# Optimization experiments

Measured on AMD Instinct MI355X. Metric: run time of the kernel, lower is better.

The kernel has to match this reference:

```python
import jax, jax.numpy as jnp
import numpy as np

DIM = 64  # matches init kwarg `dim`; temperature = sqrt(DIM)


def setup_inputs() -> dict:
    key = jax.random.key(0)
    kq, kk, kv = jax.random.split(key, 3)
    B, Lq, Lk, d = 16, 4096, 4096, DIM
    q = jax.random.normal(kq, (B, Lq, d), dtype=jnp.float32)
    k = jax.random.normal(kk, (B, Lk, d), dtype=jnp.float32)
    v = jax.random.normal(kv, (B, Lk, d), dtype=jnp.float32)
    return {"q": q, "k": k, "v": v}


def reference(q, k, v):
    # attn = softmax(q @ k^T / sqrt(dim)); dropout is identity in eval mode.
    temperature = jnp.asarray(np.sqrt(DIM), dtype=q.dtype)
    scores = jnp.einsum('bqd,bkd->bqk', q, k) / temperature  # [B, Lq, Lk]
    attn = jax.nn.softmax(scores, axis=-1)
    out = jnp.einsum('bqk,bkd->bqd', attn, v)  # [B, Lq, d]
    return out
```

## Files before the change

### kernel.cpp

```cpp
#include <hip/hip_runtime.h>
#include <stdint.h>
#include <math.h>

typedef __attribute__((ext_vector_type(2)))  float f2;
typedef __attribute__((ext_vector_type(4)))  float f4;
typedef __attribute__((ext_vector_type(16))) float f32x16;
typedef __attribute__((ext_vector_type(8)))  short bf16x8;

#define NB   16
#define LSEQ 4096
#define DH   64
#define QB   128
#define KVB  64
#define NT   (LSEQ / KVB)

__device__ __forceinline__ short f2bf(float f) {
    union { float f; uint32_t u; } v; v.f = f;
    return (short)((v.u + 0x7FFFu + ((v.u >> 16) & 1u)) >> 16);
}

__device__ __forceinline__ uint32_t cvtpk(float lo, float hi) {
    uint32_t r;
    asm("v_cvt_pk_bf16_f32 %0, %1, %2" : "=v"(r) : "v"(lo), "v"(hi));
    return r;
}

__global__ __launch_bounds__(256, 2) void fa_fwd(
    const float* __restrict__ Q, const float* __restrict__ K,
    const float* __restrict__ V, float* __restrict__ O)
{
    __shared__ __align__(16) short k_lds[2][KVB * DH];
    __shared__ __align__(16) short v_lds[2][DH * KVB];

    const int tid  = threadIdx.x;
    const int lane = tid & 63;
    const int w    = tid >> 6;
    const int l31  = lane & 31;
    const int H    = lane >> 5;

    const int b  = blockIdx.x >> 5;
    const int qt = blockIdx.x & 31;
    const int q0 = qt * QB + w * 32;

    const float* Qb = Q + (size_t)b * LSEQ * DH;
    const float* Kb = K + (size_t)b * LSEQ * DH;
    const float* Vb = V + (size_t)b * LSEQ * DH;
    float*       Ob = O + (size_t)b * LSEQ * DH;

    const float QS = 0.125f * 1.44269504088896340736f;

    bf16x8 qf[4];
#pragma unroll
    for (int kb = 0; kb < 4; ++kb) {
        const float* src = Qb + (size_t)(q0 + l31) * DH + 16 * kb + 8 * H;
        f4 a = *(const f4*)src;
        f4 c = *(const f4*)(src + 4);
        bf16x8 f;
        f[0] = f2bf(a[0] * QS); f[1] = f2bf(a[1] * QS);
        f[2] = f2bf(a[2] * QS); f[3] = f2bf(a[3] * QS);
        f[4] = f2bf(c[0] * QS); f[5] = f2bf(c[1] * QS);
        f[6] = f2bf(c[2] * QS); f[7] = f2bf(c[3] * QS);
        qf[kb] = f;
    }

    f4 kreg[4];
    f2 vreg[8];

    const int k_kv0 = (tid >> 3);
    const int k_d0  = (tid & 7) * 8;
    const int v_d0  = (tid & 31) * 2;
    const int v_g   = tid >> 5;

#define LOADK(KV0)                                                              \
    {                                                                           \
        _Pragma("unroll")                                                       \
        for (int p = 0; p < 2; ++p) {                                           \
            const float* src = Kb + (size_t)((KV0) + k_kv0 + 32 * p) * DH + k_d0; \
            kreg[2 * p]     = *(const f4*)src;                                  \
            kreg[2 * p + 1] = *(const f4*)(src + 4);                            \
        }                                                                       \
        _Pragma("unroll")                                                       \
        for (int j = 0; j < 8; ++j)                                             \
            vreg[j] = *(const f2*)&Vb[(size_t)((KV0) + 8 * v_g + j) * DH + v_d0]; \
    }

#define WRITEK(BUF)                                                             \
    {                                                                           \
        _Pragma("unroll")                                                       \
        for (int p = 0; p < 2; ++p) {                                           \
            const int kv = k_kv0 + 32 * p;                                      \
            union { bf16x8 v; uint32_t u[4]; } t;                               \
            t.u[0] = cvtpk(kreg[2 * p][0], kreg[2 * p][1]);                     \
            t.u[1] = cvtpk(kreg[2 * p][2], kreg[2 * p][3]);                     \
            t.u[2] = cvtpk(kreg[2 * p + 1][0], kreg[2 * p + 1][1]);             \
            t.u[3] = cvtpk(kreg[2 * p + 1][2], kreg[2 * p + 1][3]);             \
            *(bf16x8*)&k_lds[BUF][kv * DH + (k_d0 ^ ((kv & 7) << 3))] = t.v;    \
        }                                                                       \
        _Pragma("unroll")                                                       \
        for (int c = 0; c < 2; ++c) {                                           \
            const int d = v_d0 + c;                                             \
            union { bf16x8 v; uint32_t u[4]; } t;                               \
            t.u[0] = cvtpk(vreg[0][c], vreg[1][c]);                             \
            t.u[1] = cvtpk(vreg[2][c], vreg[3][c]);                             \
            t.u[2] = cvtpk(vreg[4][c], vreg[5][c]);                             \
            t.u[3] = cvtpk(vreg[6][c], vreg[7][c]);                             \
            *(bf16x8*)&v_lds[BUF][d * KVB + 8 * (v_g ^ (d & 7))] = t.v;         \
        }                                                                       \
    }

#define QK(BUF, D0, D1)                                                         \
    {                                                                           \
        _Pragma("unroll")                                                       \
        for (int i = 0; i < 16; ++i) { D0[i] = 0.f; D1[i] = 0.f; }              \
        _Pragma("unroll")                                                       \
        for (int kb = 0; kb < 4; ++kb) {                                        \
            const int d0 = 16 * kb + 8 * H;                                     \
            bf16x8 kf0 = *(const bf16x8*)&k_lds[BUF][(l31)      * DH + (d0 ^ ((l31 & 7) << 3))]; \
            bf16x8 kf1 = *(const bf16x8*)&k_lds[BUF][(32 + l31) * DH + (d0 ^ ((l31 & 7) << 3))]; \
            D0 = __builtin_amdgcn_mfma_f32_32x32x16_bf16(kf0, qf[kb], D0, 0, 0, 0); \
            D1 = __builtin_amdgcn_mfma_f32_32x32x16_bf16(kf1, qf[kb], D1, 0, 0, 0); \
        }                                                                       \
    }

    f32x16 oacc0, oacc1;
#pragma unroll
    for (int i = 0; i < 16; ++i) { oacc0[i] = 0.f; oacc1[i] = 0.f; }

    float l_run = 0.f;

    LOADK(0);
    WRITEK(0);
    __syncthreads();
    LOADK(KVB);

    f32x16 s0, s1;
    QK(0, s0, s1);

    for (int it = 0; it < NT; ++it) {
        const int cur = it & 1;

        float rs0 = 0.f, rs1 = 0.f, rs2 = 0.f, rs3 = 0.f;
#pragma unroll
        for (int i = 0; i < 4; ++i) {
            s0[i]      = __builtin_amdgcn_exp2f(s0[i]);      rs0 += s0[i];
            s0[i + 4]  = __builtin_amdgcn_exp2f(s0[i + 4]);  rs1 += s0[i + 4];
            s0[i + 8]  = __builtin_amdgcn_exp2f(s0[i + 8]);  rs2 += s0[i + 8];
            s0[i + 12] = __builtin_amdgcn_exp2f(s0[i + 12]); rs3 += s0[i + 12];
        }
#pragma unroll
        for (int i = 0; i < 4; ++i) {
            s1[i]      = __builtin_amdgcn_exp2f(s1[i]);      rs0 += s1[i];
            s1[i + 4]  = __builtin_amdgcn_exp2f(s1[i + 4]);  rs1 += s1[i + 4];
            s1[i + 8]  = __builtin_amdgcn_exp2f(s1[i + 8]);  rs2 += s1[i + 8];
            s1[i + 12] = __builtin_amdgcn_exp2f(s1[i + 12]); rs3 += s1[i + 12];
        }
        l_run += (rs0 + rs1) + (rs2 + rs3);

        bf16x8 pa[4];
#define MAKE_PA(P, ks2, dst)                                                    \
        {                                                                       \
            uint32_t a1 = cvtpk(P[8*(ks2)+0], P[8*(ks2)+1]);                    \
            uint32_t b1 = cvtpk(P[8*(ks2)+4], P[8*(ks2)+5]);                    \
            uint32_t a2 = cvtpk(P[8*(ks2)+2], P[8*(ks2)+3]);                    \
            uint32_t b2 = cvtpk(P[8*(ks2)+6], P[8*(ks2)+7]);                    \
            asm volatile("v_permlane32_swap_b32 %0, %1" : "+v"(a1), "+v"(b1));  \
            asm volatile("v_permlane32_swap_b32 %0, %1" : "+v"(a2), "+v"(b2));  \
            union { bf16x8 v; uint32_t u[4]; } t;                               \
            t.u[0] = a1; t.u[1] = a2; t.u[2] = b1; t.u[3] = b2;                 \
            dst = t.v;                                                          \
        }
        MAKE_PA(s0, 0, pa[0]);
        MAKE_PA(s0, 1, pa[1]);
        MAKE_PA(s1, 0, pa[2]);
        MAKE_PA(s1, 1, pa[3]);
#undef MAKE_PA

        if (it + 1 < NT) WRITEK(cur ^ 1);

        __builtin_amdgcn_s_setprio(1);
#pragma unroll
        for (int ks = 0; ks < 4; ++ks) {
            const int d0g = 2 * ks + H;
            bf16x8 vf0 = *(const bf16x8*)&v_lds[cur][(l31)      * KVB + 8 * (d0g ^ (l31 & 7))];
            bf16x8 vf1 = *(const bf16x8*)&v_lds[cur][(32 + l31) * KVB + 8 * (d0g ^ (l31 & 7))];
            oacc0 = __builtin_amdgcn_mfma_f32_32x32x16_bf16(vf0, pa[ks], oacc0, 0, 0, 0);
            oacc1 = __builtin_amdgcn_mfma_f32_32x32x16_bf16(vf1, pa[ks], oacc1, 0, 0, 0);
        }
        __builtin_amdgcn_s_setprio(0);

        if (it + 1 < NT) {
            __syncthreads();
            if (it + 2 < NT) LOADK((it + 2) * KVB);
            __builtin_amdgcn_s_setprio(1);
            QK(cur ^ 1, s0, s1);
            __builtin_amdgcn_s_setprio(0);
        }
    }

    l_run += __shfl_xor(l_run, 32);
    const float inv = 1.0f / l_run;
    const int q = q0 + l31;
#pragma unroll
    for (int k = 0; k < 4; ++k) {
        f4 o0, o1;
#pragma unroll
        for (int m = 0; m < 4; ++m) { o0[m] = oacc0[4*k+m] * inv; o1[m] = oacc1[4*k+m] * inv; }
        *(f4*)&Ob[(size_t)q * DH +      8 * k + 4 * H] = o0;
        *(f4*)&Ob[(size_t)q * DH + 32 + 8 * k + 4 * H] = o1;
    }
#undef LOADK
#undef WRITEK
#undef QK
}

extern "C" void kernel_launch(void* const* d_in, const int* in_sizes, int n_in,
                              void* d_out, int out_size, void* d_ws, size_t ws_size,
                              hipStream_t stream) {
    (void)in_sizes; (void)n_in; (void)d_ws; (void)ws_size; (void)out_size;
    const float* q = (const float*)d_in[0];
    const float* k = (const float*)d_in[1];
    const float* v = (const float*)d_in[2];
    float* o = (float*)d_out;
    hipLaunchKernelGGL(fa_fwd, dim3(NB * 32), dim3(256), 0, stream, q, k, v, o);
}
```

Before: 101.0 us.

## Compute row sums via MFMA, interleave exp with PV, remap blocks to XCDs

```diff
diff --git a/kernel.cpp b/kernel.cpp
--- a/kernel.cpp
+++ b/kernel.cpp
@@ -38,9 +38,12 @@
     const int l31  = lane & 31;
     const int H    = lane >> 5;
 
-    const int b  = blockIdx.x >> 5;
-    const int qt = blockIdx.x & 31;
-    const int q0 = qt * QB + w * 32;
+    const int bid  = blockIdx.x;
+    const int xcd  = bid & 7;
+    const int slot = bid >> 3;
+    const int b    = xcd * 2 + (slot >> 5);
+    const int qt   = slot & 31;
+    const int q0   = qt * QB + w * 32;
 
     const float* Qb = Q + (size_t)b * LSEQ * DH;
     const float* Kb = K + (size_t)b * LSEQ * DH;
@@ -63,6 +66,10 @@
         qf[kb] = f;
     }
 
+    bf16x8 ones;
+#pragma unroll
+    for (int i = 0; i < 8; ++i) ones[i] = (short)0x3F80;
+
     f4 kreg[4];
     f2 vreg[8];
 
@@ -108,25 +115,74 @@
         }                                                                       \
     }
 
-#define QK(BUF, D0, D1)                                                         \
-    {                                                                           \
-        _Pragma("unroll")                                                       \
-        for (int i = 0; i < 16; ++i) { D0[i] = 0.f; D1[i] = 0.f; }              \
+#define QKH(BUF, D, ROFF)                                                       \
+    {                                                                           \
+        _Pragma("unroll")                                                       \
+        for (int i = 0; i < 16; ++i) D[i] = 0.f;                                \
         _Pragma("unroll")                                                       \
         for (int kb = 0; kb < 4; ++kb) {                                        \
             const int d0 = 16 * kb + 8 * H;                                     \
-            bf16x8 kf0 = *(const bf16x8*)&k_lds[BUF][(l31)      * DH + (d0 ^ ((l31 & 7) << 3))]; \
-            bf16x8 kf1 = *(const bf16x8*)&k_lds[BUF][(32 + l31) * DH + (d0 ^ ((l31 & 7) << 3))]; \
-            D0 = __builtin_amdgcn_mfma_f32_32x32x16_bf16(kf0, qf[kb], D0, 0, 0, 0); \
-            D1 = __builtin_amdgcn_mfma_f32_32x32x16_bf16(kf1, qf[kb], D1, 0, 0, 0); \
-        }                                                                       \
-    }
-
-    f32x16 oacc0, oacc1;
-#pragma unroll
-    for (int i = 0; i < 16; ++i) { oacc0[i] = 0.f; oacc1[i] = 0.f; }
-
-    float l_run = 0.f;
+            bf16x8 kf = *(const bf16x8*)&k_lds[BUF][(ROFF + l31) * DH + (d0 ^ ((l31 & 7) << 3))]; \
+            D = __builtin_amdgcn_mfma_f32_32x32x16_bf16(kf, qf[kb], D, 0, 0, 0); \
+        }                                                                       \
+    }
+
+#define EXP16(S)                                                                \
+    {                                                                           \
+        _Pragma("unroll")                                                       \
+        for (int i = 0; i < 16; ++i) S[i] = __builtin_amdgcn_exp2f(S[i]);       \
+    }
+
+#define MAKE_PA(P, ks2, dst)                                                    \
+    {                                                                           \
+        uint32_t a1 = cvtpk(P[8*(ks2)+0], P[8*(ks2)+1]);                        \
+        uint32_t b1 = cvtpk(P[8*(ks2)+4], P[8*(ks2)+5]);                        \
+        uint32_t a2 = cvtpk(P[8*(ks2)+2], P[8*(ks2)+3]);                        \
+        uint32_t b2 = cvtpk(P[8*(ks2)+6], P[8*(ks2)+7]);                        \
+        asm volatile("v_permlane32_swap_b32 %0, %1" : "+v"(a1), "+v"(b1));      \
+        asm volatile("v_permlane32_swap_b32 %0, %1" : "+v"(a2), "+v"(b2));      \
+        union { bf16x8 v; uint32_t u[4]; } t;                                   \
+        t.u[0] = a1; t.u[1] = a2; t.u[2] = b1; t.u[3] = b2;                     \
+        dst = t.v;                                                              \
+    }
+
+#define PVKS(BUF, ks, pav)                                                      \
+    {                                                                           \
+        const int d0g = 2 * (ks) + H;                                           \
+        bf16x8 vf0 = *(const bf16x8*)&v_lds[BUF][(l31)      * KVB + 8 * (d0g ^ (l31 & 7))]; \
+        bf16x8 vf1 = *(const bf16x8*)&v_lds[BUF][(32 + l31) * KVB + 8 * (d0g ^ (l31 & 7))]; \
+        oacc0 = __builtin_amdgcn_mfma_f32_32x32x16_bf16(vf0, pav, oacc0, 0, 0, 0); \
+        oacc1 = __builtin_amdgcn_mfma_f32_32x32x16_bf16(vf1, pav, oacc1, 0, 0, 0); \
+        lacc  = __builtin_amdgcn_mfma_f32_32x32x16_bf16(ones, pav, lacc, 0, 0, 0); \
+    }
+
+#define BODY(IT, DO_LOAD, DO_STAGE)                                             \
+    {                                                                           \
+        const int cur = (IT) & 1;                                               \
+        bf16x8 pa0, pa1, pa2, pa3;                                              \
+        EXP16(s0);                                                              \
+        MAKE_PA(s0, 0, pa0); MAKE_PA(s0, 1, pa1);                               \
+        __builtin_amdgcn_s_setprio(1);                                          \
+        PVKS(cur, 0, pa0); PVKS(cur, 1, pa1);                                   \
+        __builtin_amdgcn_s_setprio(0);                                          \
+        EXP16(s1);                                                              \
+        MAKE_PA(s1, 0, pa2); MAKE_PA(s1, 1, pa3);                               \
+        __builtin_amdgcn_s_setprio(1);                                          \
+        PVKS(cur, 2, pa2); PVKS(cur, 3, pa3);                                   \
+        __builtin_amdgcn_s_setprio(0);                                          \
+        if (DO_STAGE) {                                                         \
+            WRITEK(cur ^ 1);                                                    \
+            __syncthreads();                                                    \
+            if (DO_LOAD) LOADK(((IT) + 2) * KVB);                               \
+            __builtin_amdgcn_s_setprio(1);                                      \
+            QKH(cur ^ 1, s0, 0); QKH(cur ^ 1, s1, 32);                          \
+            __builtin_amdgcn_s_setprio(0);                                      \
+        }                                                                       \
+    }
+
+    f32x16 oacc0, oacc1, lacc;
+#pragma unroll
+    for (int i = 0; i < 16; ++i) { oacc0[i] = 0.f; oacc1[i] = 0.f; lacc[i] = 0.f; }
 
     LOADK(0);
     WRITEK(0);
@@ -134,71 +190,14 @@
     LOADK(KVB);
 
     f32x16 s0, s1;
-    QK(0, s0, s1);
-
-    for (int it = 0; it < NT; ++it) {
-        const int cur = it & 1;
-
-        float rs0 = 0.f, rs1 = 0.f, rs2 = 0.f, rs3 = 0.f;
-#pragma unroll
-        for (int i = 0; i < 4; ++i) {
-            s0[i]      = __builtin_amdgcn_exp2f(s0[i]);      rs0 += s0[i];
-            s0[i + 4]  = __builtin_amdgcn_exp2f(s0[i + 4]);  rs1 += s0[i + 4];
-            s0[i + 8]  = __builtin_amdgcn_exp2f(s0[i + 8]);  rs2 += s0[i + 8];
-            s0[i + 12] = __builtin_amdgcn_exp2f(s0[i + 12]); rs3 += s0[i + 12];
-        }
-#pragma unroll
-        for (int i = 0; i < 4; ++i) {
-            s1[i]      = __builtin_amdgcn_exp2f(s1[i]);      rs0 += s1[i];
-            s1[i + 4]  = __builtin_amdgcn_exp2f(s1[i + 4]);  rs1 += s1[i + 4];
-            s1[i + 8]  = __builtin_amdgcn_exp2f(s1[i + 8]);  rs2 += s1[i + 8];
-            s1[i + 12] = __builtin_amdgcn_exp2f(s1[i + 12]); rs3 += s1[i + 12];
-        }
-        l_run += (rs0 + rs1) + (rs2 + rs3);
-
-        bf16x8 pa[4];
-#define MAKE_PA(P, ks2, dst)                                                    \
-        {                                                                       \
-            uint32_t a1 = cvtpk(P[8*(ks2)+0], P[8*(ks2)+1]);                    \
-            uint32_t b1 = cvtpk(P[8*(ks2)+4], P[8*(ks2)+5]);                    \
-            uint32_t a2 = cvtpk(P[8*(ks2)+2], P[8*(ks2)+3]);                    \
-            uint32_t b2 = cvtpk(P[8*(ks2)+6], P[8*(ks2)+7]);                    \
-            asm volatile("v_permlane32_swap_b32 %0, %1" : "+v"(a1), "+v"(b1));  \
-            asm volatile("v_permlane32_swap_b32 %0, %1" : "+v"(a2), "+v"(b2));  \
-            union { bf16x8 v; uint32_t u[4]; } t;                               \
-            t.u[0] = a1; t.u[1] = a2; t.u[2] = b1; t.u[3] = b2;                 \
-            dst = t.v;                                                          \
-        }
-        MAKE_PA(s0, 0, pa[0]);
-        MAKE_PA(s0, 1, pa[1]);
-        MAKE_PA(s1, 0, pa[2]);
-        MAKE_PA(s1, 1, pa[3]);
-#undef MAKE_PA
-
-        if (it + 1 < NT) WRITEK(cur ^ 1);
-
-        __builtin_amdgcn_s_setprio(1);
-#pragma unroll
-        for (int ks = 0; ks < 4; ++ks) {
-            const int d0g = 2 * ks + H;
-            bf16x8 vf0 = *(const bf16x8*)&v_lds[cur][(l31)      * KVB + 8 * (d0g ^ (l31 & 7))];
-            bf16x8 vf1 = *(const bf16x8*)&v_lds[cur][(32 + l31) * KVB + 8 * (d0g ^ (l31 & 7))];
-            oacc0 = __builtin_amdgcn_mfma_f32_32x32x16_bf16(vf0, pa[ks], oacc0, 0, 0, 0);
-            oacc1 = __builtin_amdgcn_mfma_f32_32x32x16_bf16(vf1, pa[ks], oacc1, 0, 0, 0);
-        }
-        __builtin_amdgcn_s_setprio(0);
-
-        if (it + 1 < NT) {
-            __syncthreads();
-            if (it + 2 < NT) LOADK((it + 2) * KVB);
-            __builtin_amdgcn_s_setprio(1);
-            QK(cur ^ 1, s0, s1);
-            __builtin_amdgcn_s_setprio(0);
-        }
-    }
-
-    l_run += __shfl_xor(l_run, 32);
-    const float inv = 1.0f / l_run;
+    QKH(0, s0, 0);
+    QKH(0, s1, 32);
+
+    for (int it = 0; it < NT - 2; ++it) BODY(it, 1, 1);
+    BODY(NT - 2, 0, 1);
+    BODY(NT - 1, 0, 0);
+
+    const float inv = 1.0f / lacc[0];
     const int q = q0 + l31;
 #pragma unroll
     for (int k = 0; k < 4; ++k) {
@@ -210,7 +209,11 @@
     }
 #undef LOADK
 #undef WRITEK
-#undef QK
+#undef QKH
+#undef EXP16
+#undef MAKE_PA
+#undef PVKS
+#undef BODY
 }
 
 extern "C" void kernel_launch(void* const* d_in, const int* in_sizes, int n_in,
```

Result: slower. 104.7 us (+3.6%).
